# Performance work log

Measured on AMD Instinct MI355X. Metric: run time of the kernel, lower is better.

## Reference

```python
import jax, jax.numpy as jnp
import numpy as np

B = 16384
L = 64  # num_latent
N_NODES = 13

# obs layout: [0:15] base, then per leg i: 8 hip, 8 thigh, 8 calf features
BASE_IDX = np.arange(15)
HIP_IDX = np.array([[15 + 24 * i + k for k in range(8)] for i in range(4)])
THIGH_IDX = HIP_IDX + 8
CALF_IDX = HIP_IDX + 16

# kinematic tree, bidirectional: base-hip, hip-thigh, thigh-calf
_pairs = [(0, 1), (0, 2), (0, 3), (0, 4),
          (1, 5), (2, 6), (3, 7), (4, 8),
          (5, 9), (6, 10), (7, 11), (8, 12)]
SRC = np.array([a for a, b in _pairs] + [b for a, b in _pairs])  # [24]
DST = np.array([b for a, b in _pairs] + [a for a, b in _pairs])  # [24]
LEGS = np.array([[0, 1, 5, 9], [0, 2, 6, 10], [0, 3, 7, 11], [0, 4, 8, 12]])

PARAM_SHAPES = []
for p, d in [("base", 15), ("hip", 8), ("thigh", 8), ("calf", 8)]:
    PARAM_SHAPES += [(p + "_w1", (d, 128)), (p + "_b1", (128,)),
                     (p + "_w2", (128, L)), (p + "_b2", (L,))]
for g, o in [("gn1", 2 * L), ("gn2", L)]:
    for n in ["k", "q", "v", "s"]:
        PARAM_SHAPES += [(g + "_w" + n, (2 * L, o)), (g + "_b" + n, (o,))]
PARAM_SHAPES += [("leg_w1", (4 * L, 256)), ("leg_b1", (256,)),
                 ("leg_w2", (256, 128)), ("leg_b2", (128,)),
                 ("leg_w3", (128, 3)), ("leg_b3", (3,))]


def setup_inputs() -> dict:
    key = jax.random.key(0)
    ks = jax.random.split(key, len(PARAM_SHAPES) + 2)
    inp = {"obs": jax.random.normal(ks[0], (B, 111), jnp.float32),
           "latent": jax.random.normal(ks[1], (B, N_NODES, L), jnp.float32)}
    for i, (name, shp) in enumerate(PARAM_SHAPES):
        inp[name] = jax.random.normal(ks[i + 2], shp, jnp.float32) * 0.05
    return inp


def _mlp(x, w1, b1, w2, b2):
    # Linear -> elu -> Linear (hidden [128])
    return jax.nn.elu(x @ w1 + b1) @ w2 + b2


def _res_gated_conv(x, wk, bk, wq, bq, wv, bv, ws, bs):
    # PyG ResGatedGraphConv: out_i = W_s x_i + sum_j sigmoid(W_k x_i + W_q x_j) * (W_v x_j)
    k = x @ wk + bk  # [B,N,O]
    q = x @ wq + bq
    v = x @ wv + bv
    gate = jax.nn.sigmoid(k[:, DST] + q[:, SRC])      # [B,E,O]
    msg = gate * v[:, SRC]                            # [B,E,O]
    agg = jnp.zeros_like(k).at[:, DST].add(msg)       # scatter-add to targets
    return x @ ws + bs + agg


def reference(obs, latent,
              base_w1, base_b1, base_w2, base_b2,
              hip_w1, hip_b1, hip_w2, hip_b2,
              thigh_w1, thigh_b1, thigh_w2, thigh_b2,
              calf_w1, calf_b1, calf_w2, calf_b2,
              gn1_wk, gn1_bk, gn1_wq, gn1_bq, gn1_wv, gn1_bv, gn1_ws, gn1_bs,
              gn2_wk, gn2_bk, gn2_wq, gn2_bq, gn2_wv, gn2_bv, gn2_ws, gn2_bs,
              leg_w1, leg_b1, leg_w2, leg_b2, leg_w3, leg_b3):
    b = obs.shape[0]
    base = _mlp(obs[:, BASE_IDX][:, None, :], base_w1, base_b1, base_w2, base_b2)  # [B,1,L]
    hip = _mlp(obs[:, HIP_IDX], hip_w1, hip_b1, hip_w2, hip_b2)                    # [B,4,L]
    thigh = _mlp(obs[:, THIGH_IDX], thigh_w1, thigh_b1, thigh_w2, thigh_b2)
    calf = _mlp(obs[:, CALF_IDX], calf_w1, calf_b1, calf_w2, calf_b2)
    nodes = jnp.concatenate([base, hip, thigh, calf], axis=1)                      # [B,13,L]
    h = jnp.concatenate([nodes, latent], axis=-1)                                  # [B,13,2L]
    h = jax.nn.elu(_res_gated_conv(h, gn1_wk, gn1_bk, gn1_wq, gn1_bq,
                                   gn1_wv, gn1_bv, gn1_ws, gn1_bs))
    h = _res_gated_conv(h, gn2_wk, gn2_bk, gn2_wq, gn2_bq,
                        gn2_wv, gn2_bv, gn2_ws, gn2_bs)                            # [B,13,L]
    leg_lat = h[:, LEGS].reshape(b, 4, 4 * L)                                      # [B,4,4L]
    a = jax.nn.elu(leg_lat @ leg_w1 + leg_b1)
    a = jax.nn.elu(a @ leg_w2 + leg_b2)
    a = a @ leg_w3 + leg_b3                                                        # [B,4,3]
    return a.reshape(b, 12)
```

## Files before the change

kernel.cpp:

```cpp
#include <hip/hip_runtime.h>

typedef unsigned short u16;
typedef unsigned int   u32;

#define NIN 40

struct PtrTab { const void* p[NIN]; int n[NIN]; };
struct OffsT  { int o[38]; };
struct TOffs  { int o[14]; };
struct TOffs2 { int o[12]; };

typedef __attribute__((ext_vector_type(8))) short bf16x8;
typedef __attribute__((ext_vector_type(4))) float f32x4;
#define MFMA16(a,b,c) __builtin_amdgcn_mfma_f32_16x16x32_bf16(a,b,c,0,0,0)

__device__ __forceinline__ float bf2f(u16 u){ union{u32 i; float f;} z; z.i = ((u32)u) << 16; return z.f; }
__device__ __forceinline__ u16 f2bf(float f){ union{float f; u32 i;} z; z.f = f; u32 u = z.i; return (u16)((u + 0x7fffu + ((u >> 16) & 1u)) >> 16); }
__device__ __forceinline__ float eluf(float x){ return x > 0.f ? x : (__expf(x) - 1.f); }
__device__ __forceinline__ float sigmf(float x){ return 1.f / (1.f + __expf(-x)); }

__device__ __forceinline__ float ldv(const void* p, int i, bool BF){
  if (BF){ return bf2f(((const u16*)p)[i]); }
  return ((const float*)p)[i];
}
__device__ __forceinline__ void bf8(const u16* p, float* f){
  uint4 w = *(const uint4*)(const void*)p;
  union{u32 i; float v;} t;
  t.i = w.x << 16; f[0] = t.v;  t.i = w.x & 0xffff0000u; f[1] = t.v;
  t.i = w.y << 16; f[2] = t.v;  t.i = w.y & 0xffff0000u; f[3] = t.v;
  t.i = w.z << 16; f[4] = t.v;  t.i = w.z & 0xffff0000u; f[5] = t.v;
  t.i = w.w << 16; f[6] = t.v;  t.i = w.w & 0xffff0000u; f[7] = t.v;
}
__device__ __forceinline__ void ld8(const void* p, int i, bool BF, float* f){
  if (BF){ bf8((const u16*)p + i, f); }
  else {
    const float4* q = (const float4*)(const void*)((const float*)p + i);
    float4 a = q[0], b = q[1];
    f[0]=a.x; f[1]=a.y; f[2]=a.z; f[3]=a.w; f[4]=b.x; f[5]=b.y; f[6]=b.z; f[7]=b.w;
  }
}
__device__ __forceinline__ void st8bf(u16* p, const float* f){
  u16 tmp[8];
  #pragma unroll
  for (int jj = 0; jj < 8; ++jj) tmp[jj] = f2bf(f[jj]);
  *(uint4*)(void*)p = *(const uint4*)(const void*)tmp;
}

__device__ __forceinline__ void st8_swz(u16* base, int row, int k0, const float* f){
  int byte = (row*256 + k0*2) ^ ((row & 7) << 4);
  u16 tmp[8];
  #pragma unroll
  for (int jj = 0; jj < 8; ++jj) tmp[jj] = f2bf(f[jj]);
  *(uint4*)((char*)base + byte) = *(const uint4*)(const void*)tmp;
}
__device__ __forceinline__ void st1_swz(u16* base, int row, int col, float v){
  int byte = (row*256 + col*2) ^ ((row & 7) << 4);
  *(u16*)((char*)base + byte) = f2bf(v);
}
__device__ __forceinline__ bf16x8 ldfrag(const u16* base, int row, int k0){
  int byte = (row*256 + k0*2) ^ ((row & 7) << 4);
  return *(const bf16x8*)((const char*)base + byte);
}
__device__ __forceinline__ bf16x8 ldfrag5(const u16* base, int row, int k0){
  int byte = (row*512 + k0*2) ^ ((row & 7) << 4);
  return *(const bf16x8*)((const char*)base + byte);
}
__device__ __forceinline__ void st1_5(u16* base, int row, int col, float v){
  int byte = (row*512 + col*2) ^ ((row & 7) << 4);
  *(u16*)((char*)base + byte) = f2bf(v);
}

__device__ __forceinline__ void gl16(const u16* g, u16* l){
  __builtin_amdgcn_global_load_lds((const __attribute__((address_space(1))) void*)g,
                                   (__attribute__((address_space(3))) void*)l, 16, 0, 0);
}

__device__ __forceinline__ int nbr_cnt(int n){ return n == 0 ? 4 : (n <= 8 ? 2 : 1); }
__device__ __forceinline__ int nbr_of(int n, int e){
  if (n == 0) return 1 + e;
  if (n <= 4) return e == 0 ? 0 : n + 4;
  if (n <= 8) return e == 0 ? n - 4 : n + 4;
  return n - 4;
}
__device__ __forceinline__ int prowf(int n, int r){
  return n == 0 ? 96 + r : n <= 4 ? (n-1)*8 + r : n <= 8 ? 32 + (n-5)*8 + r : 64 + (n-9)*8 + r;
}

__global__ __launch_bounds__(256) void probe_kernel(PtrTab T, int* fl){
  const int i = blockIdx.x;
  __shared__ int cnt;
  if (threadIdx.x == 0) cnt = 0;
  __syncthreads();
  int S = T.n[i]; if (S > 8192) S = 8192;
  const u16* p = (const u16*)T.p[i];
  int c = 0;
  for (int w = threadIdx.x; w < S; w += 256){
    u32 e = ((u32)p[w] >> 7) & 0xFFu;
    c += (e != 0u && (e < 96u || e > 159u)) ? 1 : 0;
  }
  atomicAdd(&cnt, c);
  __syncthreads();
  if (threadIdx.x == 0) fl[i] = (cnt > (S >> 4)) ? 0 : 1;
}

__global__ __launch_bounds__(256) void convert_kernel(PtrTab T, const int* fl, u16* dst, OffsT O){
  int s = blockIdx.x + 2;
  int j = (s >= 3 && (s & 1)) ? s - 1 : s;
  bool BF = fl[j] != 0;
  const void* src = T.p[s];
  u16* d = dst + O.o[s - 2];
  int n = T.n[s];
  for (int i = blockIdx.y * 256 + threadIdx.x; i < n; i += 1024)
    d[i] = BF ? ((const u16*)src)[i] : f2bf(((const float*)src)[i]);
}

__global__ __launch_bounds__(256) void transpose_kernel(const u16* Wb, OffsT O, u16* Wt, TOffs TF){
  static const int srcI[14] = {2,6,10,14, 16,18,20,22, 24,26,28,30, 32,34};
  static const int KK[14]   = {128,128,128,128, 128,128,128,128, 128,128,128,128, 256,256};
  static const int NNm[14]  = {64,64,64,64, 128,128,128,128, 64,64,64,64, 256,128};
  int m = blockIdx.x;
  int K = KK[m], N = NNm[m];
  const u16* src = Wb + O.o[srcI[m]];
  u16* dst = Wt + TF.o[m];
  int tot = K * N;
  for (int i = blockIdx.y * 256 + threadIdx.x; i < tot; i += 1024){
    int k = i / N, c = i % N;
    dst[c * K + k] = src[i];
  }
}

__global__ __launch_bounds__(256) void transpose2_kernel(const u16* Wb, OffsT O, u16* Wt2, TOffs2 F2){
  static const int srcI[12] = {2,6,10,14, 16,18,20,22, 24,26,28,30};
  static const int NN2[12]  = {64,64,64,64, 128,128,128,128, 64,64,64,64};
  int m = blockIdx.x;
  int N = NN2[m];
  const u16* src = Wb + O.o[srcI[m]];
  u16* dst = Wt2 + F2.o[m];
  int tot = 128 * N;
  for (int i = blockIdx.y * 256 + threadIdx.x; i < tot; i += 2048){
    int ch = i >> 11;
    int x2 = (i & 2047) * 2;
    int c  = x2 >> 8;
    int sb = x2 ^ ((c & 7) << 4);
    int scol = ch*16 + (sb >> 8);
    int sk   = (sb & 255) >> 1;
    dst[i] = src[sk * N + scol];
  }
}

__global__ __launch_bounds__(512, 4) void k1m(PtrTab T, const int* flg, const u16* Wb, OffsT O,
                                              const u16* Wt2, TOffs2 F2, u16* h2g, int Btot){
  __shared__ __attribute__((aligned(16))) u16 hidB[112*128];
  __shared__ __attribute__((aligned(16))) u16 xs  [112*128];
  __shared__ __attribute__((aligned(16))) u16 wl  [4*16*128];
  __shared__ __attribute__((aligned(16))) u16 qv  [2*104*19];
  float* obs_s = (float*)qv;

  const int tid = threadIdx.x, lane = tid & 63, wid = tid >> 6;
  const int lrow = lane & 15, lkg = lane >> 4;
  const int b0 = blockIdx.x * 8;
  const bool BFobs = flg[0] != 0, BFlat = flg[1] != 0;

  {
    uint4 z = {0,0,0,0};
    uint4* ph = (uint4*)((char*)hidB + 104*256);
    uint4* px = (uint4*)((char*)xs   + 104*256);
    for (int u = tid; u < 128; u += 512){ ph[u] = z; px[u] = z; }
  }
  for (int u = tid; u < 8*111; u += 512){
    int r = u / 111, c = u % 111;
    int br = b0 + r; if (br >= Btot) br = Btot - 1;
    obs_s[r*111 + c] = ldv(T.p[0], br*111 + c, BFobs);
  }
  __syncthreads();

  for (int u = tid; u < 13*128; u += 512){
    int n = u >> 7, rem = u & 127, r = rem >> 4, h0 = (rem & 15) << 3;
    int ty  = (n == 0) ? 0 : (n <= 4) ? 1 : (n <= 8) ? 2 : 3;
    int off = (n == 0) ? 0 : (ty == 1) ? 15 + 24*(n-1)
             : (ty == 2) ? 15 + 24*(n-5) + 8 : 15 + 24*(n-9) + 16;
    int K = (n == 0) ? 15 : 8;
    const u16* w1 = Wb + O.o[4*ty];
    float acc8[8]; bf8(Wb + O.o[4*ty+1] + h0, acc8);
    for (int k = 0; k < K; ++k){
      float xv = obs_s[r*111 + off + k];
      float wf[8]; bf8(w1 + k*128 + h0, wf);
      #pragma unroll
      for (int jj = 0; jj < 8; ++jj) acc8[jj] = fmaf(xv, wf[jj], acc8[jj]);
    }
    #pragma unroll
    for (int jj = 0; jj < 8; ++jj) acc8[jj] = eluf(acc8[jj]);
    st8_swz(hidB, prowf(n, r), h0, acc8);
  }
  for (int u = tid; u < 13*64; u += 512){
    int n = u >> 6, rem = u & 63, r = rem >> 3, j0 = (rem & 7) << 3;
    int br = b0 + r; if (br >= Btot) br = Btot - 1;
    float lv[8]; ld8(T.p[1], (br*13 + n)*64 + j0, BFlat, lv);
    st8_swz(xs, n*8 + r, 64 + j0, lv);
  }
  __syncthreads();

  bf16x8 axf[4];

  if (wid < 7){
    #pragma unroll
    for (int kk = 0; kk < 4; ++kk) axf[kk] = ldfrag(hidB, wid*16 + lrow, kk*32 + lkg*8);
  }
  for (int c0 = 0; c0 < 64; c0 += 16){
    #pragma unroll
    for (int j = 0; j < 2; ++j){
      int u = tid + j*512, m = u >> 8, um = u & 255;
      gl16(Wt2 + F2.o[m] + (c0 >> 4)*2048 + um*8, wl + m*2048 + (um & 192)*8);
    }
    __syncthreads();
    if (wid < 7){
      int t = wid;
      int tyt = t < 2 ? 1 : t < 4 ? 2 : t < 6 ? 3 : 0;
      f32x4 d = {0.f,0.f,0.f,0.f};
      #pragma unroll
      for (int kk = 0; kk < 4; ++kk){
        bf16x8 b = ldfrag(wl + tyt*2048, lrow, kk*32 + lkg*8);
        d = MFMA16(axf[kk], b, d);
      }
      int c2 = c0 + lrow;
      float bb = bf2f(Wb[O.o[4*tyt+3] + c2]);
      #pragma unroll
      for (int i = 0; i < 4; ++i){
        int prow = t*16 + lkg*4 + i;
        if (prow < 104){
          int n = prow < 32 ? 1 + (prow >> 3) : prow < 64 ? 5 + ((prow-32) >> 3)
                : prow < 96 ? 9 + ((prow-64) >> 3) : 0;
          st1_swz(xs, n*8 + (prow & 7), c2, d[i] + bb);
        }
      }
    }
    __syncthreads();
  }

  #pragma unroll
  for (int j = 0; j < 2; ++j){
    int u = tid + j*512, m = u >> 8, um = u & 255;
    gl16(Wt2 + F2.o[4+m] + um*8, wl + m*2048 + (um & 192)*8);
  }
  __syncthreads();

  if (wid < 7){
    #pragma unroll
    for (int kk = 0; kk < 4; ++kk) axf[kk] = ldfrag(xs, wid*16 + lrow, kk*32 + lkg*8);
  }
  {
    const u16* bk = Wb + O.o[17]; const u16* bq = Wb + O.o[19];
    const u16* bv = Wb + O.o[21]; const u16* bs = Wb + O.o[23];
    for (int ch = 0; ch < 8; ++ch){
      int c0 = ch * 16;
      f32x4 kacc = {0.f,0.f,0.f,0.f}, sacc = {0.f,0.f,0.f,0.f};
      if (wid < 7){
        int t = wid;
        #pragma unroll
        for (int m = 0; m < 4; ++m){
          f32x4 d = {0.f,0.f,0.f,0.f};
          #pragma unroll
          for (int kk = 0; kk < 4; ++kk){
            bf16x8 b = ldfrag(wl + m*2048, lrow, kk*32 + lkg*8);
            d = MFMA16(axf[kk], b, d);
          }
          if (m == 0) kacc = d;
          else if (m == 3) sacc = d;
          else {
            #pragma unroll
            for (int i = 0; i < 4; ++i){
              int gr = t*16 + lkg*4 + i;
              if (gr < 104) qv[(m-1)*1976 + gr*19 + lrow] = f2bf(d[i]);
            }
          }
        }
      }
      __syncthreads();
      #pragma unroll
      for (int j = 0; j < 2; ++j){
        int u = tid + j*512, m = u >> 8, um = u & 255;
        const u16* g = (ch < 7) ? Wt2 + F2.o[4+m] + (ch+1)*2048 + um*8
                                : Wt2 + F2.o[8+m] + um*8;
        gl16(g, wl + m*2048 + (um & 192)*8);
      }
      if (wid < 7){
        int t = wid, c = c0 + lrow;
        float bkq = bf2f(bk[c]) + bf2f(bq[c]);
        float bvv = bf2f(bv[c]);
        float bss = bf2f(bs[c]);
        #pragma unroll
        for (int i = 0; i < 4; ++i){
          int gr = t*16 + lkg*4 + i;
          if (gr < 104){
            int n = gr >> 3, rr = gr & 7;
            float acc = sacc[i] + bss;
            float kk_ = kacc[i] + bkq;
            int cnt = nbr_cnt(n);
            for (int e = 0; e < cnt; ++e){
              int s = nbr_of(n, e);
              float ql = bf2f(qv[(s*8 + rr)*19 + lrow]);
              float vl = bf2f(qv[1976 + (s*8 + rr)*19 + lrow]);
              acc += sigmf(kk_ + ql) * (vl + bvv);
            }
            st1_swz(hidB, gr, c, eluf(acc));
          }
        }
      }
      __syncthreads();
    }
  }

  if (wid < 7){
    #pragma unroll
    for (int kk = 0; kk < 4; ++kk) axf[kk] = ldfrag(hidB, wid*16 + lrow, kk*32 + lkg*8);
  }
  {
    const u16* bk = Wb + O.o[25]; const u16* bq = Wb + O.o[27];
    const u16* bv = Wb + O.o[29]; const u16* bs = Wb + O.o[31];
    for (int ch = 0; ch < 4; ++ch){
      int c0 = ch * 16;
      f32x4 kacc = {0.f,0.f,0.f,0.f}, sacc = {0.f,0.f,0.f,0.f};
      if (wid < 7){
        int t = wid;
        #pragma unroll
        for (int m = 0; m < 4; ++m){
          f32x4 d = {0.f,0.f,0.f,0.f};
          #pragma unroll
          for (int kk = 0; kk < 4; ++kk){
            bf16x8 b = ldfrag(wl + m*2048, lrow, kk*32 + lkg*8);
            d = MFMA16(axf[kk], b, d);
          }
          if (m == 0) kacc = d;
          else if (m == 3) sacc = d;
          else {
            #pragma unroll
            for (int i = 0; i < 4; ++i){
              int gr = t*16 + lkg*4 + i;
              if (gr < 104) qv[(m-1)*1976 + gr*19 + lrow] = f2bf(d[i]);
            }
          }
        }
      }
      __syncthreads();
      if (ch < 3){
        #pragma unroll
        for (int j = 0; j < 2; ++j){
          int u = tid + j*512, m = u >> 8, um = u & 255;
          gl16(Wt2 + F2.o[8+m] + (ch+1)*2048 + um*8, wl + m*2048 + (um & 192)*8);
        }
      }
      if (wid < 7){
        int t = wid, c = c0 + lrow;
        float bkq = bf2f(bk[c]) + bf2f(bq[c]);
        float bvv = bf2f(bv[c]);
        float bss = bf2f(bs[c]);
        #pragma unroll
        for (int i = 0; i < 4; ++i){
          int gr = t*16 + lkg*4 + i;
          if (gr < 104){
            int n = gr >> 3, rr = gr & 7;
            float acc = sacc[i] + bss;
            float kk_ = kacc[i] + bkq;
            int cnt = nbr_cnt(n);
            for (int e = 0; e < cnt; ++e){
              int s = nbr_of(n, e);
              float ql = bf2f(qv[(s*8 + rr)*19 + lrow]);
              float vl = bf2f(qv[1976 + (s*8 + rr)*19 + lrow]);
              acc += sigmf(kk_ + ql) * (vl + bvv);
            }
            xs[gr*128 + c] = f2bf(acc);
          }
        }
      }
      __syncthreads();
    }
  }

  for (int u = tid; u < 104*8; u += 512){
    int gr = u >> 3, j0 = (u & 7) << 3;
    int n = gr >> 3, rr = gr & 7;
    if (b0 + rr < Btot)
      *(uint4*)(h2g + ((b0 + rr)*13 + n)*64 + j0) = *(const uint4*)(xs + gr*128 + j0);
  }
}

__global__ __launch_bounds__(512) void k2m(const u16* Wb, OffsT O, const u16* Wt, TOffs TF,
                                           const u16* h2g, float* out, int Btot){
  __shared__ u16 lat [64*256];
  __shared__ u16 a1s [64*256];
  __shared__ u16 a2s [64*128];
  __shared__ u16 wbuf[2][32*256];

  const int tid  = threadIdx.x;
  const int lane = tid & 63;
  const int wid  = tid >> 6;
  const int lrow = lane & 15;
  const int lkg  = lane >> 4;
  const int r0   = blockIdx.x * 16;
  const int mt   = wid >> 1, cb = wid & 1;

  for (int u = tid; u < 64*32; u += 512){
    int inst = u >> 5, k0 = (u & 31) << 3;
    int r = inst >> 2, g = inst & 3;
    int br = r0 + r; if (br >= Btot) br = Btot - 1;
    int seg = k0 >> 6, f = k0 & 63;
    int node = (seg == 0) ? 0 : (seg - 1)*4 + 1 + g;
    uint4 v = *(const uint4*)(h2g + (br*13 + node)*64 + f);
    *(uint4*)((char*)lat + ((inst*512 + k0*2) ^ ((inst&7)<<4))) = v;
  }
  const u16* w1t = Wt + TF.o[12];
  const u16* b1  = Wb + O.o[33];
  for (int u = tid; u < 1024; u += 512){
    int c = u >> 5, kg = (u & 31) << 3;
    uint4 v = *(const uint4*)(w1t + c*256 + kg);
    *(uint4*)((char*)wbuf[0] + ((c*512 + kg*2) ^ ((c&7)<<4))) = v;
  }
  __syncthreads();

  for (int ch = 0; ch < 8; ++ch){
    if (ch < 7){
      for (int u = tid; u < 1024; u += 512){
        int c = u >> 5, kg = (u & 31) << 3;
        uint4 v = *(const uint4*)(w1t + ((ch+1)*32 + c)*256 + kg);
        *(uint4*)((char*)wbuf[(ch+1)&1] + ((c*512 + kg*2) ^ ((c&7)<<4))) = v;
      }
    }
    const u16* wb = wbuf[ch&1];
    f32x4 d = {0.f,0.f,0.f,0.f};
    #pragma unroll
    for (int kk = 0; kk < 8; ++kk){
      bf16x8 a = ldfrag5(lat, mt*16 + lrow, kk*32 + lkg*8);
      bf16x8 b = ldfrag5(wb,  cb*16 + lrow, kk*32 + lkg*8);
      d = MFMA16(a, b, d);
    }
    int col = ch*32 + cb*16 + lrow;
    float bvv = bf2f(b1[col]);
    #pragma unroll
    for (int i = 0; i < 4; ++i)
      st1_5(a1s, mt*16 + lkg*4 + i, col, eluf(d[i] + bvv));
    __syncthreads();
  }

  const u16* w2t = Wt + TF.o[13];
  const u16* b2  = Wb + O.o[35];
  for (int u = tid; u < 1024; u += 512){
    int c = u >> 5, kg = (u & 31) << 3;
    uint4 v = *(const uint4*)(w2t + c*256 + kg);
    *(uint4*)((char*)wbuf[0] + ((c*512 + kg*2) ^ ((c&7)<<4))) = v;
  }
  __syncthreads();
  for (int ch = 0; ch < 4; ++ch){
    if (ch < 3){
      for (int u = tid; u < 1024; u += 512){
        int c = u >> 5, kg = (u & 31) << 3;
        uint4 v = *(const uint4*)(w2t + ((ch+1)*32 + c)*256 + kg);
        *(uint4*)((char*)wbuf[(ch+1)&1] + ((c*512 + kg*2) ^ ((c&7)<<4))) = v;
      }
    }
    const u16* wb = wbuf[ch&1];
    f32x4 d = {0.f,0.f,0.f,0.f};
    #pragma unroll
    for (int kk = 0; kk < 8; ++kk){
      bf16x8 a = ldfrag5(a1s, mt*16 + lrow, kk*32 + lkg*8);
      bf16x8 b = ldfrag5(wb,  cb*16 + lrow, kk*32 + lkg*8);
      d = MFMA16(a, b, d);
    }
    int col = ch*32 + cb*16 + lrow;
    float bvv = bf2f(b2[col]);
    #pragma unroll
    for (int i = 0; i < 4; ++i)
      st1_swz(a2s, mt*16 + lkg*4 + i, col, eluf(d[i] + bvv));
    __syncthreads();
  }

  if (tid < 64*3){
    const u16* w3 = Wb + O.o[36], *b3 = Wb + O.o[37];
    int inst = tid / 3, c = tid % 3;
    int r = inst >> 2, g = inst & 3;
    float acc = bf2f(b3[c]);
    for (int k0 = 0; k0 < 128; k0 += 8){
      const u16* ap = (const u16*)((const char*)a2s + ((inst*256 + k0*2) ^ ((inst&7)<<4)));
      float av[8]; bf8(ap, av);
      #pragma unroll
      for (int jj = 0; jj < 8; ++jj) acc = fmaf(av[jj], bf2f(w3[(k0+jj)*3 + c]), acc);
    }
    if (r0 + r < Btot) out[(r0 + r)*12 + g*3 + c] = acc;
  }
}

#define TPB 512
#define RR  6
__global__ __launch_bounds__(TPB) void actor_v2(PtrTab T, const int* flg, float* out, int Btot){
  __shared__ float A [RR][13][132];
  __shared__ float Bf[RR][13][132];
  __shared__ u16   Cq[3][RR][13][128];
  __shared__ float obs_s[RR][111];
  __shared__ int   fls[NIN];

  const int tid = threadIdx.x;
  const int b0  = blockIdx.x * RR;

  if (tid < NIN){ int j = (tid >= 3 && (tid & 1)) ? tid - 1 : tid; fls[tid] = flg[j]; }
  __syncthreads();
  const bool BFobs = fls[0] != 0, BFlat = fls[1] != 0;

  for (int u = tid; u < RR * 111; u += TPB){
    int r = u / 111, c = u % 111;
    int br = b0 + r; if (br >= Btot) br = Btot - 1;
    obs_s[r][c] = ldv(T.p[0], br * 111 + c, BFobs);
  }
  __syncthreads();

  for (int u = tid; u < RR * 13 * 16; u += TPB){
    int r = u / 208, rem = u % 208, n = rem >> 4, h0 = (rem & 15) << 3;
    int ty  = (n == 0) ? 0 : (n <= 4) ? 1 : (n <= 8) ? 2 : 3;
    int off = (n == 0) ? 0 : (ty == 1) ? 15 + 24 * (n - 1)
             : (ty == 2) ? 15 + 24 * (n - 5) + 8 : 15 + 24 * (n - 9) + 16;
    int K = (n == 0) ? 15 : 8;
    const void* w1 = T.p[2 + 4 * ty];
    bool bw = fls[2 + 4 * ty] != 0, bb = fls[3 + 4 * ty] != 0;
    float acc8[8]; ld8(T.p[3 + 4 * ty], h0, bb, acc8);
    for (int k = 0; k < K; ++k){
      float xv = obs_s[r][off + k];
      float wf[8]; ld8(w1, k * 128 + h0, bw, wf);
      #pragma unroll
      for (int jj = 0; jj < 8; ++jj) acc8[jj] = fmaf(xv, wf[jj], acc8[jj]);
    }
    #pragma unroll
    for (int jj = 0; jj < 8; ++jj) Bf[r][n][h0 + jj] = eluf(acc8[jj]);
  }
  __syncthreads();

  for (int u = tid; u < 13 * 8; u += TPB){
    int n = u >> 3, o0 = (u & 7) << 3;
    int ty = (n == 0) ? 0 : (n <= 4) ? 1 : (n <= 8) ? 2 : 3;
    const void* w2 = T.p[4 + 4 * ty];
    bool bw = fls[4 + 4 * ty] != 0, bb = fls[5 + 4 * ty] != 0;
    float bv[8]; ld8(T.p[5 + 4 * ty], o0, bb, bv);
    float acc[RR][8];
    #pragma unroll
    for (int r = 0; r < RR; ++r)
      #pragma unroll
      for (int jj = 0; jj < 8; ++jj) acc[r][jj] = bv[jj];
    #pragma unroll 4
    for (int k = 0; k < 128; ++k){
      float wf[8]; ld8(w2, k * 64 + o0, bw, wf);
      #pragma unroll
      for (int r = 0; r < RR; ++r){
        float xv = Bf[r][n][k];
        #pragma unroll
        for (int jj = 0; jj < 8; ++jj) acc[r][jj] = fmaf(xv, wf[jj], acc[r][jj]);
      }
    }
    #pragma unroll
    for (int r = 0; r < RR; ++r)
      #pragma unroll
      for (int jj = 0; jj < 8; ++jj) A[r][n][o0 + jj] = acc[r][jj];
  }
  for (int u = tid; u < RR * 13 * 8; u += TPB){
    int r = u / 104, rem = u % 104, n = rem >> 3, j0 = (rem & 7) << 3;
    int br = b0 + r; if (br >= Btot) br = Btot - 1;
    float lv[8]; ld8(T.p[1], (br * 13 + n) * 64 + j0, BFlat, lv);
    #pragma unroll
    for (int jj = 0; jj < 8; ++jj) A[r][n][64 + j0 + jj] = lv[jj];
  }
  __syncthreads();

  for (int u = tid; u < 4 * 13 * 16; u += TPB){
    int mat = u / 208, rem = u % 208, n = rem >> 4, j0 = (rem & 15) << 3;
    const void* W = T.p[18 + 2 * mat];
    bool bw = fls[18 + 2 * mat] != 0, bb = fls[19 + 2 * mat] != 0;
    float bv[8]; ld8(T.p[19 + 2 * mat], j0, bb, bv);
    float acc[RR][8];
    #pragma unroll
    for (int r = 0; r < RR; ++r)
      #pragma unroll
      for (int jj = 0; jj < 8; ++jj) acc[r][jj] = bv[jj];
    #pragma unroll 4
    for (int k = 0; k < 128; ++k){
      float wf[8]; ld8(W, k * 128 + j0, bw, wf);
      #pragma unroll
      for (int r = 0; r < RR; ++r){
        float xv = A[r][n][k];
        #pragma unroll
        for (int jj = 0; jj < 8; ++jj) acc[r][jj] = fmaf(xv, wf[jj], acc[r][jj]);
      }
    }
    if (mat < 3){
      #pragma unroll
      for (int r = 0; r < RR; ++r) st8bf(&Cq[mat][r][n][j0], acc[r]);
    } else {
      #pragma unroll
      for (int r = 0; r < RR; ++r)
        #pragma unroll
        for (int jj = 0; jj < 8; ++jj) Bf[r][n][j0 + jj] = acc[r][jj];
    }
  }
  __syncthreads();

  for (int u = tid; u < RR * 13 * 16; u += TPB){
    int r = u / 208, rem = u % 208, n = rem >> 4, j0 = (rem & 15) << 3;
    float acc8[8];
    #pragma unroll
    for (int jj = 0; jj < 8; ++jj) acc8[jj] = Bf[r][n][j0 + jj];
    float k8[8]; bf8(&Cq[0][r][n][j0], k8);
    int cnt = nbr_cnt(n);
    for (int e = 0; e < cnt; ++e){
      int s = nbr_of(n, e);
      float q8[8], v8[8];
      bf8(&Cq[1][r][s][j0], q8);
      bf8(&Cq[2][r][s][j0], v8);
      #pragma unroll
      for (int jj = 0; jj < 8; ++jj) acc8[jj] = fmaf(sigmf(k8[jj] + q8[jj]), v8[jj], acc8[jj]);
    }
    #pragma unroll
    for (int jj = 0; jj < 8; ++jj) Bf[r][n][j0 + jj] = eluf(acc8[jj]);
  }
  __syncthreads();

  for (int u = tid; u < 4 * 13 * 8; u += TPB){
    int mat = u / 104, rem = u % 104, n = rem >> 3, j0 = (rem & 7) << 3;
    const void* W = T.p[26 + 2 * mat];
    bool bw = fls[26 + 2 * mat] != 0, bb = fls[27 + 2 * mat] != 0;
    float bv[8]; ld8(T.p[27 + 2 * mat], j0, bb, bv);
    float acc[RR][8];
    #pragma unroll
    for (int r = 0; r < RR; ++r)
      #pragma unroll
      for (int jj = 0; jj < 8; ++jj) acc[r][jj] = bv[jj];
    #pragma unroll 4
    for (int k = 0; k < 128; ++k){
      float wf[8]; ld8(W, k * 64 + j0, bw, wf);
      #pragma unroll
      for (int r = 0; r < RR; ++r){
        float xv = Bf[r][n][k];
        #pragma unroll
        for (int jj = 0; jj < 8; ++jj) acc[r][jj] = fmaf(xv, wf[jj], acc[r][jj]);
      }
    }
    if (mat < 3){
      #pragma unroll
      for (int r = 0; r < RR; ++r) st8bf(&Cq[mat][r][n][j0], acc[r]);
    } else {
      #pragma unroll
      for (int r = 0; r < RR; ++r)
        #pragma unroll
        for (int jj = 0; jj < 8; ++jj) A[r][n][j0 + jj] = acc[r][jj];
    }
  }
  __syncthreads();

  for (int u = tid; u < RR * 13 * 8; u += TPB){
    int r = u / 104, rem = u % 104, n = rem >> 3, j0 = (rem & 7) << 3;
    float acc8[8];
    #pragma unroll
    for (int jj = 0; jj < 8; ++jj) acc8[jj] = A[r][n][j0 + jj];
    float k8[8]; bf8(&Cq[0][r][n][j0], k8);
    int cnt = nbr_cnt(n);
    for (int e = 0; e < cnt; ++e){
      int s = nbr_of(n, e);
      float q8[8], v8[8];
      bf8(&Cq[1][r][s][j0], q8);
      bf8(&Cq[2][r][s][j0], v8);
      #pragma unroll
      for (int jj = 0; jj < 8; ++jj) acc8[jj] = fmaf(sigmf(k8[jj] + q8[jj]), v8[jj], acc8[jj]);
    }
    #pragma unroll
    for (int jj = 0; jj < 8; ++jj) A[r][n][j0 + jj] = acc8[jj];
  }
  __syncthreads();

  float* a1f = (float*)&Cq[0][0][0][0];
  float* a2f = (float*)&Bf[0][0][0];
  {
    bool bw = fls[34] != 0, bb = fls[35] != 0;
    for (int u = tid; u < 6 * 32; u += TPB){
      int iq = u >> 5, j0 = (u & 31) << 3;
      float bv[8]; ld8(T.p[35], j0, bb, bv);
      float acc[4][8];
      #pragma unroll
      for (int t = 0; t < 4; ++t)
        #pragma unroll
        for (int jj = 0; jj < 8; ++jj) acc[t][jj] = bv[jj];
      #pragma unroll 2
      for (int k = 0; k < 256; ++k){
        float wf[8]; ld8(T.p[34], k * 256 + j0, bw, wf);
        int seg = k >> 6, f = k & 63;
        #pragma unroll
        for (int t = 0; t < 4; ++t){
          int inst = iq * 4 + t, r = inst >> 2, g = inst & 3;
          int node = (seg == 0) ? 0 : (seg - 1) * 4 + 1 + g;
          float xv = A[r][node][f];
          #pragma unroll
          for (int jj = 0; jj < 8; ++jj) acc[t][jj] = fmaf(xv, wf[jj], acc[t][jj]);
        }
      }
      #pragma unroll
      for (int t = 0; t < 4; ++t){
        int inst = iq * 4 + t;
        #pragma unroll
        for (int jj = 0; jj < 8; ++jj) a1f[inst * 256 + j0 + jj] = eluf(acc[t][jj]);
      }
    }
  }
  __syncthreads();
  {
    bool bw = fls[36] != 0, bb = fls[37] != 0;
    for (int u = tid; u < 6 * 16; u += TPB){
      int iq = u >> 4, j0 = (u & 15) << 3;
      float bv[8]; ld8(T.p[37], j0, bb, bv);
      float acc[4][8];
      #pragma unroll
      for (int t = 0; t < 4; ++t)
        #pragma unroll
        for (int jj = 0; jj < 8; ++jj) acc[t][jj] = bv[jj];
      #pragma unroll 2
      for (int k = 0; k < 256; ++k){
        float wf[8]; ld8(T.p[36], k * 128 + j0, bw, wf);
        #pragma unroll
        for (int t = 0; t < 4; ++t){
          float xv = a1f[(iq * 4 + t) * 256 + k];
          #pragma unroll
          for (int jj = 0; jj < 8; ++jj) acc[t][jj] = fmaf(xv, wf[jj], acc[t][jj]);
        }
      }
      #pragma unroll
      for (int t = 0; t < 4; ++t){
        int inst = iq * 4 + t;
        #pragma unroll
        for (int jj = 0; jj < 8; ++jj) a2f[inst * 128 + j0 + jj] = eluf(acc[t][jj]);
      }
    }
  }
  __syncthreads();
  if (tid < RR * 4 * 3){
    int inst = tid / 3, c = tid % 3;
    int r = inst >> 2, g = inst & 3;
    bool bw = fls[38] != 0, bb = fls[39] != 0;
    float acc = ldv(T.p[39], c, bb);
    for (int k = 0; k < 128; ++k) acc = fmaf(a2f[inst * 128 + k], ldv(T.p[38], k * 3 + c, bw), acc);
    if (b0 + r < Btot) out[(b0 + r) * 12 + g * 3 + c] = acc;
  }
}

extern "C" void kernel_launch(void* const* d_in, const int* in_sizes, int n_in,
                              void* d_out, int out_size, void* d_ws, size_t ws_size,
                              hipStream_t stream){
  (void)out_size;
  PtrTab T;
  for (int i = 0; i < NIN; ++i){
    T.p[i] = (i < n_in) ? d_in[i] : d_in[0];
    T.n[i] = (i < n_in) ? in_sizes[i] : 1;
  }
  int* fl = (int*)d_ws;
  hipLaunchKernelGGL(probe_kernel, dim3(NIN), dim3(256), 0, stream, T, fl);

  int Btot = T.n[0] / 111;

  OffsT O;
  size_t acc = 0;
  for (int s = 0; s < 38; ++s){
    O.o[s] = (int)acc;
    acc += ((size_t)T.n[s + 2] + 7) & ~(size_t)7;
  }
  static const int KK[14] = {128,128,128,128, 128,128,128,128, 128,128,128,128, 256,256};
  static const int NNm[14]= {64,64,64,64, 128,128,128,128, 64,64,64,64, 256,128};
  TOffs TF;
  int wtElems = 0;
  for (int m = 0; m < 14; ++m){ TF.o[m] = wtElems; wtElems += KK[m]*NNm[m]; }
  static const int NN2[12] = {64,64,64,64, 128,128,128,128, 64,64,64,64};
  TOffs2 F2;
  int w2Elems = 0;
  for (int m = 0; m < 12; ++m){ F2.o[m] = w2Elems; w2Elems += 128*NN2[m]; }

  size_t wtoff  = ((256 + acc * 2 + 511) / 512) * 512;
  size_t wt2off = ((wtoff + (size_t)wtElems * 2 + 511) / 512) * 512;
  size_t h2off  = ((wt2off + (size_t)w2Elems * 2 + 511) / 512) * 512;
  size_t need   = h2off + (size_t)Btot * 832 * 2;

  if (ws_size >= need){
    u16* Wb  = (u16*)((char*)d_ws + 256);
    u16* Wt  = (u16*)((char*)d_ws + wtoff);
    u16* Wt2 = (u16*)((char*)d_ws + wt2off);
    u16* h2g = (u16*)((char*)d_ws + h2off);
    hipLaunchKernelGGL(convert_kernel, dim3(38, 4), dim3(256), 0, stream, T, fl, Wb, O);
    hipLaunchKernelGGL(transpose_kernel, dim3(14, 4), dim3(256), 0, stream, Wb, O, Wt, TF);
    hipLaunchKernelGGL(transpose2_kernel, dim3(12, 8), dim3(256), 0, stream, Wb, O, Wt2, F2);
    hipLaunchKernelGGL(k1m, dim3((unsigned)((Btot + 7) / 8)), dim3(512), 0, stream,
                       T, fl, Wb, O, Wt2, F2, h2g, Btot);
    hipLaunchKernelGGL(k2m, dim3((unsigned)((Btot + 15) / 16)), dim3(512), 0, stream,
                       Wb, O, Wt, TF, h2g, (float*)d_out, Btot);
  } else {
    hipLaunchKernelGGL(actor_v2, dim3((unsigned)((Btot + RR - 1) / RR)), dim3(TPB), 0, stream,
                       T, fl, (float*)d_out, Btot);
  }
}
```

Before: 318.1 us.

## Double-buffer weight chunks in LDS by reusing dead activation buffers

Weight chunks for the node-MLP second layer and both graph-conv layers are now prefetched one chunk ahead. The next chunk goes into an alternate LDS buffer, reusing hidB or xs once their activations have been moved into registers. Global-to-LDS weight copies for chunk ch+1 are issued before the MFMA work on chunk ch, which removes one barrier-separated load phase per chunk. The risk is aliasing: the activation buffers must not be read or written while they hold weights, and extra barriers were added at the phase boundaries to guard this.

```diff
diff --git a/kernel.cpp b/kernel.cpp
--- a/kernel.cpp
+++ b/kernel.cpp
@@ -162,6 +162,13 @@
   const bool BFobs = flg[0] != 0, BFlat = flg[1] != 0;
 
   {
+    #pragma unroll
+    for (int j = 0; j < 2; ++j){
+      int u = tid + j*512, m = u >> 8, um = u & 255;
+      gl16(Wt2 + F2.o[m] + um*8, wl + m*2048 + (um & 192)*8);
+    }
+  }
+  {
     uint4 z = {0,0,0,0};
     uint4* ph = (uint4*)((char*)hidB + 104*256);
     uint4* px = (uint4*)((char*)xs   + 104*256);
@@ -206,23 +213,32 @@
     #pragma unroll
     for (int kk = 0; kk < 4; ++kk) axf[kk] = ldfrag(hidB, wid*16 + lrow, kk*32 + lkg*8);
   }
-  for (int c0 = 0; c0 < 64; c0 += 16){
+  __syncthreads();
+  for (int ch = 0; ch < 4; ++ch){
     #pragma unroll
     for (int j = 0; j < 2; ++j){
       int u = tid + j*512, m = u >> 8, um = u & 255;
-      gl16(Wt2 + F2.o[m] + (c0 >> 4)*2048 + um*8, wl + m*2048 + (um & 192)*8);
-    }
-    __syncthreads();
+      const u16* g; u16* dst;
+      if (ch < 3){
+        g = Wt2 + F2.o[m] + (ch+1)*2048 + um*8;
+        dst = (((ch+1) & 1) ? hidB : wl) + m*2048 + (um & 192)*8;
+      } else {
+        g = Wt2 + F2.o[4+m] + um*8;
+        dst = wl + m*2048 + (um & 192)*8;
+      }
+      gl16(g, dst);
+    }
+    const u16* wb = (ch & 1) ? hidB : wl;
     if (wid < 7){
       int t = wid;
       int tyt = t < 2 ? 1 : t < 4 ? 2 : t < 6 ? 3 : 0;
       f32x4 d = {0.f,0.f,0.f,0.f};
       #pragma unroll
       for (int kk = 0; kk < 4; ++kk){
-        bf16x8 b = ldfrag(wl + tyt*2048, lrow, kk*32 + lkg*8);
+        bf16x8 b = ldfrag(wb + tyt*2048, lrow, kk*32 + lkg*8);
         d = MFMA16(axf[kk], b, d);
       }
-      int c2 = c0 + lrow;
+      int c2 = ch*16 + lrow;
       float bb = bf2f(Wb[O.o[4*tyt+3] + c2]);
       #pragma unroll
       for (int i = 0; i < 4; ++i){
@@ -237,21 +253,29 @@
     __syncthreads();
   }
 
-  #pragma unroll
-  for (int j = 0; j < 2; ++j){
-    int u = tid + j*512, m = u >> 8, um = u & 255;
-    gl16(Wt2 + F2.o[4+m] + um*8, wl + m*2048 + (um & 192)*8);
-  }
-  __syncthreads();
-
   if (wid < 7){
     #pragma unroll
     for (int kk = 0; kk < 4; ++kk) axf[kk] = ldfrag(xs, wid*16 + lrow, kk*32 + lkg*8);
   }
+  __syncthreads();
   {
     const u16* bk = Wb + O.o[17]; const u16* bq = Wb + O.o[19];
     const u16* bv = Wb + O.o[21]; const u16* bs = Wb + O.o[23];
     for (int ch = 0; ch < 8; ++ch){
+      #pragma unroll
+      for (int j = 0; j < 2; ++j){
+        int u = tid + j*512, m = u >> 8, um = u & 255;
+        const u16* g; u16* dst;
+        if (ch < 7){
+          g = Wt2 + F2.o[4+m] + (ch+1)*2048 + um*8;
+          dst = (((ch+1) & 1) ? xs : wl) + m*2048 + (um & 192)*8;
+        } else {
+          g = Wt2 + F2.o[8+m] + um*8;
+          dst = wl + m*2048 + (um & 192)*8;
+        }
+        gl16(g, dst);
+      }
+      const u16* wb = (ch & 1) ? xs : wl;
       int c0 = ch * 16;
       f32x4 kacc = {0.f,0.f,0.f,0.f}, sacc = {0.f,0.f,0.f,0.f};
       if (wid < 7){
@@ -261,7 +285,7 @@
           f32x4 d = {0.f,0.f,0.f,0.f};
           #pragma unroll
           for (int kk = 0; kk < 4; ++kk){
-            bf16x8 b = ldfrag(wl + m*2048, lrow, kk*32 + lkg*8);
+            bf16x8 b = ldfrag(wb + m*2048, lrow, kk*32 + lkg*8);
             d = MFMA16(axf[kk], b, d);
           }
           if (m == 0) kacc = d;
@@ -276,13 +300,6 @@
         }
       }
       __syncthreads();
-      #pragma unroll
-      for (int j = 0; j < 2; ++j){
-        int u = tid + j*512, m = u >> 8, um = u & 255;
-        const u16* g = (ch < 7) ? Wt2 + F2.o[4+m] + (ch+1)*2048 + um*8
-                                : Wt2 + F2.o[8+m] + um*8;
-        gl16(g, wl + m*2048 + (um & 192)*8);
-      }
       if (wid < 7){
         int t = wid, c = c0 + lrow;
         float bkq = bf2f(bk[c]) + bf2f(bq[c]);
@@ -314,10 +331,20 @@
     #pragma unroll
     for (int kk = 0; kk < 4; ++kk) axf[kk] = ldfrag(hidB, wid*16 + lrow, kk*32 + lkg*8);
   }
+  __syncthreads();
   {
     const u16* bk = Wb + O.o[25]; const u16* bq = Wb + O.o[27];
     const u16* bv = Wb + O.o[29]; const u16* bs = Wb + O.o[31];
     for (int ch = 0; ch < 4; ++ch){
+      if (ch < 3){
+        #pragma unroll
+        for (int j = 0; j < 2; ++j){
+          int u = tid + j*512, m = u >> 8, um = u & 255;
+          u16* dst = (((ch+1) & 1) ? hidB : wl) + m*2048 + (um & 192)*8;
+          gl16(Wt2 + F2.o[8+m] + (ch+1)*2048 + um*8, dst);
+        }
+      }
+      const u16* wb = (ch & 1) ? hidB : wl;
       int c0 = ch * 16;
       f32x4 kacc = {0.f,0.f,0.f,0.f}, sacc = {0.f,0.f,0.f,0.f};
       if (wid < 7){
@@ -327,7 +354,7 @@
           f32x4 d = {0.f,0.f,0.f,0.f};
           #pragma unroll
           for (int kk = 0; kk < 4; ++kk){
-            bf16x8 b = ldfrag(wl + m*2048, lrow, kk*32 + lkg*8);
+            bf16x8 b = ldfrag(wb + m*2048, lrow, kk*32 + lkg*8);
             d = MFMA16(axf[kk], b, d);
           }
           if (m == 0) kacc = d;
@@ -342,13 +369,6 @@
         }
       }
       __syncthreads();
-      if (ch < 3){
-        #pragma unroll
-        for (int j = 0; j < 2; ++j){
-          int u = tid + j*512, m = u >> 8, um = u & 255;
-          gl16(Wt2 + F2.o[8+m] + (ch+1)*2048 + um*8, wl + m*2048 + (um & 192)*8);
-        }
-      }
       if (wid < 7){
         int t = wid, c = c0 + lrow;
         float bkq = bf2f(bk[c]) + bf2f(bq[c]);
```

Result: no change. 320.6 us (+0.8%).
